# Kernel optimization log

Measured on AMD Instinct MI355X. Metric: run time of the kernel, lower is better.

## Reference

```python
import jax, jax.numpy as jnp
import numpy as np

T, B, IN, H, OUT = 128, 1024, 47, 646, 5

def setup_inputs() -> dict:
    key = jax.random.key(0)
    ks = jax.random.split(key, 11)
    s_in = 1.0 / np.sqrt(H)
    return {
        "xs": jax.random.normal(ks[0], (T, B, IN), dtype=jnp.float32),
        "W_ih0": jax.random.normal(ks[1], (H, IN), dtype=jnp.float32) * s_in,
        "W_hh0": jax.random.normal(ks[2], (H, H), dtype=jnp.float32) * s_in,
        "b_ih0": jax.random.normal(ks[3], (H,), dtype=jnp.float32) * s_in,
        "b_hh0": jax.random.normal(ks[4], (H,), dtype=jnp.float32) * s_in,
        "W_ih1": jax.random.normal(ks[5], (H, H), dtype=jnp.float32) * s_in,
        "W_hh1": jax.random.normal(ks[6], (H, H), dtype=jnp.float32) * s_in,
        "b_ih1": jax.random.normal(ks[7], (H,), dtype=jnp.float32) * s_in,
        "b_hh1": jax.random.normal(ks[8], (H,), dtype=jnp.float32) * s_in,
        "W_out": jax.random.normal(ks[9], (OUT, H), dtype=jnp.float32) * s_in,
        "b_out": jnp.zeros((OUT,), dtype=jnp.float32),
    }

def reference(xs, W_ih0, W_hh0, b_ih0, b_hh0, W_ih1, W_hh1, b_ih1, b_hh1, W_out, b_out):
    batch = xs.shape[1]
    h0 = jnp.zeros((batch, H), dtype=xs.dtype)
    h1 = jnp.zeros((batch, H), dtype=xs.dtype)

    def step(carry, x_t):
        h0, h1 = carry
        # layer 0: Elman cell, tanh
        h0 = jnp.tanh(x_t @ W_ih0.T + b_ih0 + h0 @ W_hh0.T + b_hh0)
        # layer 1 consumes layer 0's output at this timestep
        h1 = jnp.tanh(h0 @ W_ih1.T + b_ih1 + h1 @ W_hh1.T + b_hh1)
        return (h0, h1), None

    (h0, h1), _ = jax.lax.scan(step, (h0, h1), xs)
    # classifier on last layer's final hidden state
    logits = h1 @ W_out.T + b_out  # [B, 5]
    return logits
```

## Files before the change

### kernel.cpp

```cpp
#include <hip/hip_runtime.h>
#include <hip/hip_bf16.h>

#define T_STEPS 128
#define B_SZ    1024
#define IN_SZ   47
#define H_SZ    646
#define OUT_SZ  5

#define XK    96
#define K0    768
#define K1    1344
#define N0PAD 704
#define N1PAD 672
#define RING  17
#define SLAB  172032
#define FSTR  160

#define NL0B  7
#define NL1B  14
#define NBLK  (8 * (NL0B + NL1B))

typedef __hip_bfloat16 bf16;
typedef unsigned short ush;
using frag8 = __attribute__((ext_vector_type(8))) short;
using f32x4 = __attribute__((ext_vector_type(4))) float;


__global__ void prep_xs(const float* __restrict__ xs, bf16* __restrict__ xs_pad) {
    int idx = blockIdx.x * blockDim.x + threadIdx.x;
    if (idx >= T_STEPS * B_SZ * XK) return;
    int k = idx % XK;
    int rb = idx / XK;
    float v = (k < IN_SZ) ? xs[(size_t)rb * IN_SZ + k] : 0.f;
    xs_pad[idx] = __float2bfloat16(v);
}

__global__ void pack_w0(const float* __restrict__ Wih, const float* __restrict__ Whh,
                        bf16* __restrict__ Wc) {
    int idx = blockIdx.x * blockDim.x + threadIdx.x;
    if (idx >= N0PAD * K0) return;
    int j = idx / K0, k = idx % K0;
    float v = 0.f;
    if (j < H_SZ) {
        if (k < IN_SZ)                      v = Wih[(size_t)j * IN_SZ + k];
        else if (k >= XK && k < XK + H_SZ)  v = Whh[(size_t)j * H_SZ + (k - XK)];
    }
    Wc[idx] = __float2bfloat16(v);
}

__global__ void pack_w1(const float* __restrict__ Wih, const float* __restrict__ Whh,
                        bf16* __restrict__ Wc) {
    int idx = blockIdx.x * blockDim.x + threadIdx.x;
    if (idx >= N1PAD * K1) return;
    int j = idx / K1, k = idx % K1;
    float v = 0.f;
    if (j < H_SZ) {
        if (k < H_SZ)                          v = Wih[(size_t)j * H_SZ + k];
        else if (k >= 672 && k < 672 + H_SZ)   v = Whh[(size_t)j * H_SZ + (k - 672)];
    }
    Wc[idx] = __float2bfloat16(v);
}

__global__ void pack_bias(const float* __restrict__ bi, const float* __restrict__ bh,
                          float* __restrict__ b, int n) {
    int j = blockIdx.x * blockDim.x + threadIdx.x;
    if (j >= n) return;
    b[j] = (j < H_SZ) ? (bi[j] + bh[j]) : 0.f;
}


__device__ __forceinline__ void tanh_store(ush* dst, float x) {
    x = fminf(fmaxf(x, -15.f), 15.f);
    float e = __expf(2.f * x);
    bf16 hb = __float2bfloat16((e - 1.f) / (e + 1.f));
    __hip_atomic_store(dst, *(ush*)&hb, __ATOMIC_RELAXED, __HIP_MEMORY_SCOPE_AGENT);
}

__device__ __forceinline__ void poll_ge(int* p, int need) {
    while (__hip_atomic_load(p, __ATOMIC_RELAXED, __HIP_MEMORY_SCOPE_AGENT) < need)
        __builtin_amdgcn_s_sleep(1);
}

__global__ __launch_bounds__(512, 2) void persist(
    const bf16* __restrict__ xs_pad, const bf16* __restrict__ Wc0,
    const bf16* __restrict__ Wc1, const float* __restrict__ b0,
    const float* __restrict__ b1, bf16* __restrict__ Sring,
    int* __restrict__ flags)
{
    extern __shared__ ush Wlds[];
    const int bid  = blockIdx.x;
    const int rg   = bid & 7;
    const int c8   = bid >> 3;
    const bool isL0 = (c8 < NL0B);
    const int tid  = threadIdx.x;
    const int wv   = tid >> 6;
    const int lane = tid & 63;
    const int q8   = (lane >> 4) * 8;
    const int l15  = lane & 15;

    if (isL0) {
        const int col0 = c8 * 96;
        for (int g = wv; g < 144; g += 8) {
            int kc = g / 6, ct = g % 6;
            const bf16* src = Wc0 + (size_t)(col0 + ct*16 + l15) * K0 + kc*32 + q8;
            *(uint4*)&Wlds[g*512 + lane*8] = *(const uint4*)src;
        }
    } else {
        const int col0 = (c8 - NL0B) * 48;
        for (int g = wv; g < 126; g += 8) {
            int kc = g / 3, ct = g % 3;
            const bf16* src = Wc1 + (size_t)(col0 + ct*16 + l15) * K1 + kc*32 + q8;
            *(uint4*)&Wlds[g*512 + lane*8] = *(const uint4*)src;
        }
    }
    __syncthreads();

    const int loc = wv * 16 + l15;
    bf16* const ringbase = Sring + (size_t)rg * RING * SLAB;
    int*  const fL0 = flags + rg * FSTR;
    int*  const fL1 = flags + (8 + rg) * FSTR;

    if (isL0) {
        const int col0 = c8 * 96;
        float bias[6];
        #pragma unroll
        for (int ct = 0; ct < 6; ++ct) bias[ct] = b0[col0 + ct*16 + l15];

        for (int p = 0; p < 128; ++p) {
            if (tid == 0) {
                if (p > 0)   poll_ge(&fL0[p-1], NL0B);
                if (p >= 17) poll_ge(&fL1[p-16], NL1B);
            }
            __syncthreads();
            if (p >= RING + 1 && (p - 1) % RING == 0)
                __builtin_amdgcn_fence(__ATOMIC_ACQUIRE, "agent");
            const bf16* rsl = ringbase + (size_t)((p + RING - 1) % RING) * SLAB;
            bf16*       wsl = ringbase + (size_t)(p % RING) * SLAB;

            const bf16* xr = xs_pad + ((size_t)p * B_SZ + rg*128 + loc) * XK + q8;
            const bf16* hr = rsl + (size_t)loc * K1 + q8;
            uint4 abuf[24];
            #pragma unroll
            for (int i = 0; i < 24; ++i)
                abuf[i] = (i < 3) ? *(const uint4*)(xr + i*32)
                                  : *(const uint4*)(hr + (i-3)*32);
            f32x4 acc[6] = {};
            #pragma unroll
            for (int kc = 0; kc < 24; ++kc) {
                frag8 af = *(const frag8*)&abuf[kc];
                #pragma unroll
                for (int ct = 0; ct < 6; ++ct) {
                    frag8 wf = *(const frag8*)&Wlds[(kc*6+ct)*512 + lane*8];
                    acc[ct] = __builtin_amdgcn_mfma_f32_16x16x32_bf16(
                        af, wf, acc[ct], 0, 0, 0);
                }
            }
            const int rbase = wv*16 + (lane>>4)*4;
            #pragma unroll
            for (int ct = 0; ct < 6; ++ct) {
                const int col = col0 + ct*16 + l15;
                if (col < H_SZ) {
                    #pragma unroll
                    for (int i = 0; i < 4; ++i)
                        tanh_store((ush*)(wsl + (size_t)(rbase+i)*K1 + col),
                                   acc[ct][i] + bias[ct]);
                }
            }
            __syncthreads();
            if (tid == 0)
                __hip_atomic_fetch_add(&fL0[p], 1, __ATOMIC_RELAXED,
                                       __HIP_MEMORY_SCOPE_AGENT);
        }
    } else {
        const int col0 = (c8 - NL0B) * 48;
        float bias[3];
        #pragma unroll
        for (int ct = 0; ct < 3; ++ct) bias[ct] = b1[col0 + ct*16 + l15];

        for (int q = 1; q <= 128; ++q) {
            if (tid == 0) {
                poll_ge(&fL0[q-1], NL0B);
                if (q > 1) poll_ge(&fL1[q-1], NL1B);
            }
            __syncthreads();
            if (q >= RING + 1 && (q - 1) % RING == 0)
                __builtin_amdgcn_fence(__ATOMIC_ACQUIRE, "agent");
            const bf16* rsl = ringbase + (size_t)((q + RING - 1) % RING) * SLAB;
            bf16*       wsl = ringbase + (size_t)(q % RING) * SLAB;

            const bf16* ar = rsl + (size_t)loc * K1 + q8;
            uint4 abuf[42];
            #pragma unroll
            for (int i = 0; i < 42; ++i) abuf[i] = *(const uint4*)(ar + i*32);
            f32x4 acc[3] = {};
            #pragma unroll
            for (int kc = 0; kc < 42; ++kc) {
                frag8 af = *(const frag8*)&abuf[kc];
                #pragma unroll
                for (int ct = 0; ct < 3; ++ct) {
                    frag8 wf = *(const frag8*)&Wlds[(kc*3+ct)*512 + lane*8];
                    acc[ct] = __builtin_amdgcn_mfma_f32_16x16x32_bf16(
                        af, wf, acc[ct], 0, 0, 0);
                }
            }
            const int rbase = wv*16 + (lane>>4)*4;
            #pragma unroll
            for (int ct = 0; ct < 3; ++ct) {
                const int col = col0 + ct*16 + l15;
                if (col < H_SZ) {
                    #pragma unroll
                    for (int i = 0; i < 4; ++i)
                        tanh_store((ush*)(wsl + (size_t)(rbase+i)*K1 + 672 + col),
                                   acc[ct][i] + bias[ct]);
                }
            }
            __syncthreads();
            if (tid == 0)
                __hip_atomic_fetch_add(&fL1[q], 1, __ATOMIC_RELAXED,
                                       __HIP_MEMORY_SCOPE_AGENT);
        }
    }
}

__global__ __launch_bounds__(256) void classifier(
    const bf16* __restrict__ Sring, const float* __restrict__ Wout,
    const float* __restrict__ bout, float* __restrict__ out)
{
    const int wave = threadIdx.x >> 6, lane = threadIdx.x & 63;
    const int row = blockIdx.x * 4 + wave;
    const int rg = row >> 7, loc = row & 127;
    const bf16* h1 = Sring + ((size_t)rg * RING + (128 % RING)) * SLAB
                     + (size_t)loc * K1 + 672;
    float acc[OUT_SZ] = {0.f, 0.f, 0.f, 0.f, 0.f};
    for (int k = lane; k < H_SZ; k += 64) {
        float h = __bfloat162float(h1[k]);
        #pragma unroll
        for (int o = 0; o < OUT_SZ; ++o) acc[o] += h * Wout[(size_t)o * H_SZ + k];
    }
    #pragma unroll
    for (int o = 0; o < OUT_SZ; ++o) {
        float v = acc[o];
        #pragma unroll
        for (int off = 32; off; off >>= 1) v += __shfl_down(v, off, 64);
        if (lane == 0) out[(size_t)row * OUT_SZ + o] = v + bout[o];
    }
}


extern "C" void kernel_launch(void* const* d_in, const int* in_sizes, int n_in,
                              void* d_out, int out_size, void* d_ws, size_t ws_size,
                              hipStream_t stream) {
    const float* xs   = (const float*)d_in[0];
    const float* Wih0 = (const float*)d_in[1];
    const float* Whh0 = (const float*)d_in[2];
    const float* bih0 = (const float*)d_in[3];
    const float* bhh0 = (const float*)d_in[4];
    const float* Wih1 = (const float*)d_in[5];
    const float* Whh1 = (const float*)d_in[6];
    const float* bih1 = (const float*)d_in[7];
    const float* bhh1 = (const float*)d_in[8];
    const float* Wout = (const float*)d_in[9];
    const float* bout = (const float*)d_in[10];
    float* out = (float*)d_out;

    char* ws = (char*)d_ws;
    size_t off = 0;
    bf16* xs_pad = (bf16*)(ws + off); off += (size_t)T_STEPS * B_SZ * XK * 2;
    bf16* Wc0    = (bf16*)(ws + off); off += (size_t)N0PAD * K0 * 2;
    bf16* Wc1    = (bf16*)(ws + off); off += (size_t)N1PAD * K1 * 2;
    float* b0    = (float*)(ws + off); off += (size_t)N0PAD * 4;
    float* b1    = (float*)(ws + off); off += (size_t)N1PAD * 4;
    bf16* Sring  = (bf16*)(ws + off); off += (size_t)8 * RING * SLAB * 2;
    int*  flags  = (int*)(ws + off);  off += (size_t)16 * FSTR * 4;

    hipMemsetAsync(Sring, 0, (size_t)8 * RING * SLAB * 2, stream);
    hipMemsetAsync(flags, 0, (size_t)16 * FSTR * 4, stream);

    prep_xs <<<(T_STEPS * B_SZ * XK + 255) / 256, 256, 0, stream>>>(xs, xs_pad);
    pack_w0 <<<(N0PAD * K0 + 255) / 256, 256, 0, stream>>>(Wih0, Whh0, Wc0);
    pack_w1 <<<(N1PAD * K1 + 255) / 256, 256, 0, stream>>>(Wih1, Whh1, Wc1);
    pack_bias<<<(N0PAD + 255) / 256, 256, 0, stream>>>(bih0, bhh0, b0, N0PAD);
    pack_bias<<<(N1PAD + 255) / 256, 256, 0, stream>>>(bih1, bhh1, b1, N1PAD);

    hipFuncSetAttribute((const void*)persist,
                        hipFuncAttributeMaxDynamicSharedMemorySize, 147456);
    void* args[] = { (void*)&xs_pad, (void*)&Wc0, (void*)&Wc1, (void*)&b0,
                     (void*)&b1, (void*)&Sring, (void*)&flags };
    hipLaunchCooperativeKernel((const void*)persist, dim3(NBLK), dim3(512),
                               args, 147456, stream);

    classifier<<<B_SZ / 4, 256, 0, stream>>>(Sring, Wout, bout, out);
}
```

Before: 1.661 ms.

## Replace block-level barriers with per-wave flags for finer-grained cross-block sync

Each wave now signals and polls its own flag counters, indexed by row group and wave, instead of one thread per block syncing through __syncthreads. This is meant to let waves handling different 16-row slices advance independently and drop the two block barriers per timestep. The layer-0 x-input loads are also hoisted ahead of the poll so they overlap the wait. It relies on a wave only reading the rows written by the same-index wave in other blocks, and it uses eight times more flag memory and eight times more atomic traffic.

```diff
diff --git a/kernel.cpp b/kernel.cpp
--- a/kernel.cpp
+++ b/kernel.cpp
@@ -117,8 +117,8 @@
 
     const int loc = wv * 16 + l15;
     bf16* const ringbase = Sring + (size_t)rg * RING * SLAB;
-    int*  const fL0 = flags + rg * FSTR;
-    int*  const fL1 = flags + (8 + rg) * FSTR;
+    int* const fL0s = flags + ((0*8 + rg)*8 + wv) * FSTR;
+    int* const fL1s = flags + ((1*8 + rg)*8 + wv) * FSTR;
 
     if (isL0) {
         const int col0 = c8 * 96;
@@ -127,27 +127,31 @@
         for (int ct = 0; ct < 6; ++ct) bias[ct] = b0[col0 + ct*16 + l15];
 
         for (int p = 0; p < 128; ++p) {
-            if (tid == 0) {
-                if (p > 0)   poll_ge(&fL0[p-1], NL0B);
-                if (p >= 17) poll_ge(&fL1[p-16], NL1B);
-            }
-            __syncthreads();
+            const bf16* rsl = ringbase + (size_t)((p + RING - 1) % RING) * SLAB;
+            bf16*       wsl = ringbase + (size_t)(p % RING) * SLAB;
+
+            const bf16* xr = xs_pad + ((size_t)p * B_SZ + rg*128 + loc) * XK + q8;
+            uint4 xbuf[3];
+            #pragma unroll
+            for (int i = 0; i < 3; ++i) xbuf[i] = *(const uint4*)(xr + i*32);
+
+            if (lane == 0) {
+                if (p > 0)   poll_ge(&fL0s[p-1], NL0B);
+                if (p >= 17) poll_ge(&fL1s[p-16], NL1B);
+            }
             if (p >= RING + 1 && (p - 1) % RING == 0)
                 __builtin_amdgcn_fence(__ATOMIC_ACQUIRE, "agent");
-            const bf16* rsl = ringbase + (size_t)((p + RING - 1) % RING) * SLAB;
-            bf16*       wsl = ringbase + (size_t)(p % RING) * SLAB;
-
-            const bf16* xr = xs_pad + ((size_t)p * B_SZ + rg*128 + loc) * XK + q8;
+
             const bf16* hr = rsl + (size_t)loc * K1 + q8;
-            uint4 abuf[24];
-            #pragma unroll
-            for (int i = 0; i < 24; ++i)
-                abuf[i] = (i < 3) ? *(const uint4*)(xr + i*32)
-                                  : *(const uint4*)(hr + (i-3)*32);
+            uint4 hbuf[21];
+            #pragma unroll
+            for (int i = 0; i < 21; ++i) hbuf[i] = *(const uint4*)(hr + i*32);
+
             f32x4 acc[6] = {};
             #pragma unroll
             for (int kc = 0; kc < 24; ++kc) {
-                frag8 af = *(const frag8*)&abuf[kc];
+                frag8 af = (kc < 3) ? *(const frag8*)&xbuf[kc]
+                                    : *(const frag8*)&hbuf[kc-3];
                 #pragma unroll
                 for (int ct = 0; ct < 6; ++ct) {
                     frag8 wf = *(const frag8*)&Wlds[(kc*6+ct)*512 + lane*8];
@@ -166,9 +170,9 @@
                                    acc[ct][i] + bias[ct]);
                 }
             }
-            __syncthreads();
-            if (tid == 0)
-                __hip_atomic_fetch_add(&fL0[p], 1, __ATOMIC_RELAXED,
+            __builtin_amdgcn_s_waitcnt(0);
+            if (lane == 0)
+                __hip_atomic_fetch_add(&fL0s[p], 1, __ATOMIC_RELAXED,
                                        __HIP_MEMORY_SCOPE_AGENT);
         }
     } else {
@@ -178,15 +182,15 @@
         for (int ct = 0; ct < 3; ++ct) bias[ct] = b1[col0 + ct*16 + l15];
 
         for (int q = 1; q <= 128; ++q) {
-            if (tid == 0) {
-                poll_ge(&fL0[q-1], NL0B);
-                if (q > 1) poll_ge(&fL1[q-1], NL1B);
-            }
-            __syncthreads();
+            const bf16* rsl = ringbase + (size_t)((q + RING - 1) % RING) * SLAB;
+            bf16*       wsl = ringbase + (size_t)(q % RING) * SLAB;
+
+            if (lane == 0) {
+                poll_ge(&fL0s[q-1], NL0B);
+                if (q > 1) poll_ge(&fL1s[q-1], NL1B);
+            }
             if (q >= RING + 1 && (q - 1) % RING == 0)
                 __builtin_amdgcn_fence(__ATOMIC_ACQUIRE, "agent");
-            const bf16* rsl = ringbase + (size_t)((q + RING - 1) % RING) * SLAB;
-            bf16*       wsl = ringbase + (size_t)(q % RING) * SLAB;
 
             const bf16* ar = rsl + (size_t)loc * K1 + q8;
             uint4 abuf[42];
@@ -214,9 +218,9 @@
                                    acc[ct][i] + bias[ct]);
                 }
             }
-            __syncthreads();
-            if (tid == 0)
-                __hip_atomic_fetch_add(&fL1[q], 1, __ATOMIC_RELAXED,
+            __builtin_amdgcn_s_waitcnt(0);
+            if (lane == 0)
+                __hip_atomic_fetch_add(&fL1s[q], 1, __ATOMIC_RELAXED,
                                        __HIP_MEMORY_SCOPE_AGENT);
         }
     }
@@ -271,10 +275,10 @@
     float* b0    = (float*)(ws + off); off += (size_t)N0PAD * 4;
     float* b1    = (float*)(ws + off); off += (size_t)N1PAD * 4;
     bf16* Sring  = (bf16*)(ws + off); off += (size_t)8 * RING * SLAB * 2;
-    int*  flags  = (int*)(ws + off);  off += (size_t)16 * FSTR * 4;
+    int*  flags  = (int*)(ws + off);  off += (size_t)128 * FSTR * 4;
 
     hipMemsetAsync(Sring, 0, (size_t)8 * RING * SLAB * 2, stream);
-    hipMemsetAsync(flags, 0, (size_t)16 * FSTR * 4, stream);
+    hipMemsetAsync(flags, 0, (size_t)128 * FSTR * 4, stream);
 
     prep_xs <<<(T_STEPS * B_SZ * XK + 255) / 256, 256, 0, stream>>>(xs, xs_pad);
     pack_w0 <<<(N0PAD * K0 + 255) / 256, 256, 0, stream>>>(Wih0, Whh0, Wc0);
```

Result: slower. 1.757 ms (+5.8%).
